# Optimization experiments

Hardware: AMD Instinct MI355X
Metric: run time of the kernel (lower is better)

The kernel has to match this reference:

```python
import jax, jax.numpy as jnp
from jax import lax
import numpy as np

RADIUS = 0.2
NSAMPLE = 64


def setup_inputs() -> dict:
    key = jax.random.key(0)
    k1, k2, k3 = jax.random.split(key, 3)
    B, N, S, C = 4, 16384, 4096, 64
    xyz = jax.random.uniform(k1, (B, N, 3), dtype=jnp.float32)
    new_xyz = jax.random.uniform(k2, (B, S, 3), dtype=jnp.float32)
    features = jax.random.normal(k3, (B, C, N), dtype=jnp.float32)
    return {"xyz": xyz, "new_xyz": new_xyz, "features": features}


def _ball_query(xyz, new_xyz, radius, nsample):
    # xyz: (B,N,3), new_xyz: (B,S,3) -> idx (B,S,nsample) int32
    # Squared distances via GEMM form: ||q||^2 + ||p||^2 - 2 q.p
    N = xyz.shape[1]
    q2 = jnp.sum(new_xyz * new_xyz, axis=-1)            # (B,S)
    p2 = jnp.sum(xyz * xyz, axis=-1)                    # (B,N)
    qp = jnp.einsum('bsd,bnd->bsn', new_xyz, xyz)       # (B,S,N)
    d2 = q2[:, :, None] + p2[:, None, :] - 2.0 * qp     # (B,S,N)
    # CUDA ball_query semantics: take the FIRST nsample points (by index order)
    # within radius; pad remaining slots with the first found index; 0 if none.
    cand = jnp.where(d2 < radius * radius,
                     jnp.arange(N, dtype=jnp.int32), jnp.int32(N))  # (B,S,N)
    neg_smallest, _ = lax.top_k(-cand, nsample)         # nsample smallest indices
    idx = -neg_smallest                                 # ascending (B,S,nsample)
    first = idx[..., :1]
    idx = jnp.where(idx == N, first, idx)               # pad with first neighbor
    idx = jnp.where(idx == N, 0, idx)                   # no neighbor at all -> 0
    return idx


def _group(feat, idx):
    # feat: (B,C,N), idx: (B,S,K) -> (B,C,S,K)
    return jax.vmap(lambda f, i: f[:, i])(feat, idx)


def reference(xyz, new_xyz, features):
    idx = _ball_query(xyz, new_xyz, RADIUS, NSAMPLE)        # (B,S,K)
    grouped_xyz = _group(jnp.transpose(xyz, (0, 2, 1)), idx)  # (B,3,S,K)
    grouped_xyz = grouped_xyz - jnp.transpose(new_xyz, (0, 2, 1))[..., None]
    grouped_features = _group(features, idx)                # (B,C,S,K)
    return jnp.concatenate([grouped_xyz, grouped_features], axis=1)  # (B,3+C,S,K)
```

## Files before the change

### kernel.cpp

```cpp
#include <hip/hip_runtime.h>
#include <cstdint>
#include <cstddef>

#define BB 4
#define NN 16384
#define SS 4096
#define CC 64
#define NSAMP 64
#define R2 0.04f

#define TRANS_BLOCKS (BB * (NN / 64))
#define XYZW_BLOCKS  64

typedef float f32x4 __attribute__((ext_vector_type(4)));

__global__ __launch_bounds__(256) void prep_kernel(const float* __restrict__ xyz,
                                                   const float* __restrict__ feat,
                                                   float* __restrict__ featT,
                                                   f32x4* __restrict__ xyzw) {
    int t = threadIdx.x;
    if (blockIdx.x < TRANS_BLOCKS) {
        __shared__ float tile[64][65];
        int blk = blockIdx.x;
        int b   = blk / (NN / 64);
        int n0  = (blk % (NN / 64)) * 64;
        int nl  = t & 63;
        int cq  = t >> 6;
#pragma unroll
        for (int p = 0; p < 16; ++p) {
            int c = cq + p * 4;
            tile[c][nl] = feat[((size_t)b * CC + c) * NN + n0 + nl];
        }
        __syncthreads();
#pragma unroll
        for (int p = 0; p < 16; ++p) {
            int nl2 = cq + p * 4;
            featT[((size_t)b * NN + n0 + nl2) * CC + nl] = tile[nl][nl2];
        }
        return;
    }
    int T0     = (blockIdx.x - TRANS_BLOCKS) * 256 + t;
    int stride = XYZW_BLOCKS * 256;
    for (int p = T0; p < BB * NN; p += stride) {
        float x = xyz[(size_t)p * 3 + 0];
        float y = xyz[(size_t)p * 3 + 1];
        float z = xyz[(size_t)p * 3 + 2];
        f32x4 o = {x, y, z, 0.0f};
        xyzw[p] = o;
    }
}

__global__ __launch_bounds__(256) void fused_qg(const f32x4* __restrict__ xyzw,
                                                const float* __restrict__ nxyz,
                                                const float* __restrict__ featT,
                                                float* __restrict__ out) {
    __shared__ float sub[4][64][17];
    __shared__ int   sidx[4][NSAMP];

    int t    = threadIdx.x;
    int wid  = t >> 6;
    int lane = t & 63;
    int wg   = blockIdx.x;
    int qblk = (wg & 7) * (BB * SS / 8 / 4) + (wg >> 3);
    int q    = qblk * 4 + wid;
    int b    = q >> 12;
    int s    = q & (SS - 1);

    const f32x4* xp = xyzw + (size_t)b * NN;
    float qx = nxyz[((size_t)b * SS + s) * 3 + 0];
    float qy = nxyz[((size_t)b * SS + s) * 3 + 1];
    float qz = nxyz[((size_t)b * SS + s) * 3 + 2];
    float q2 = __fadd_rn(__fadd_rn(__fmul_rn(qx, qx), __fmul_rn(qy, qy)),
                         __fmul_rn(qz, qz));

    int cnt = 0;
    f32x4 A  = xp[lane];
    f32x4 Bv = xp[lane + 64];
    for (int base = 0; base < NN; base += 128) {
        f32x4 ca = A, cb = Bv;
        int nb = base + 128;
        if (nb < NN) {
            A  = xp[nb + lane];
            Bv = xp[nb + 64 + lane];
        }
        float p2a = __fadd_rn(__fadd_rn(__fmul_rn(ca.x, ca.x), __fmul_rn(ca.y, ca.y)),
                              __fmul_rn(ca.z, ca.z));
        float qpa = __fadd_rn(__fadd_rn(__fmul_rn(qx, ca.x), __fmul_rn(qy, ca.y)),
                              __fmul_rn(qz, ca.z));
        float d2a = __fsub_rn(__fadd_rn(q2, p2a), __fadd_rn(qpa, qpa));
        float p2b = __fadd_rn(__fadd_rn(__fmul_rn(cb.x, cb.x), __fmul_rn(cb.y, cb.y)),
                              __fmul_rn(cb.z, cb.z));
        float qpb = __fadd_rn(__fadd_rn(__fmul_rn(qx, cb.x), __fmul_rn(qy, cb.y)),
                              __fmul_rn(qz, cb.z));
        float d2b = __fsub_rn(__fadd_rn(q2, p2b), __fadd_rn(qpb, qpb));
        bool in0 = d2a < R2;
        bool in1 = d2b < R2;
        unsigned long long m0 = __ballot(in0);
        unsigned long long m1 = __ballot(in1);
        int c0 = __popcll(m0);
        if (in0) {
            int pos = cnt + __popcll(m0 & ((1ull << lane) - 1ull));
            if (pos < NSAMP) sidx[wid][pos] = base + lane;
        }
        if (in1) {
            int pos = cnt + c0 + __popcll(m1 & ((1ull << lane) - 1ull));
            if (pos < NSAMP) sidx[wid][pos] = base + 64 + lane;
        }
        cnt += c0 + __popcll(m1);
        if (cnt >= NSAMP) break;
    }
    asm volatile("s_waitcnt lgkmcnt(0)" ::: "memory");
    int total = cnt < NSAMP ? cnt : NSAMP;
    int myidx = (total == 0) ? 0 : ((lane < total) ? sidx[wid][lane] : sidx[wid][0]);
    asm volatile("s_waitcnt lgkmcnt(0)" ::: "memory");
    sidx[wid][lane] = myidx;
    asm volatile("s_waitcnt lgkmcnt(0)" ::: "memory");

    size_t obase = ((size_t)b * 67) * SS * 64 + (size_t)s * 64;
    size_t chs   = (size_t)SS * 64;

    {
        const f32x4 P = xp[myidx];
        float gx = __fsub_rn(P.x, qx);
        float gy = __fsub_rn(P.y, qy);
        float gz = __fsub_rn(P.z, qz);
        __builtin_nontemporal_store(gx, out + obase + 0 * chs + lane);
        __builtin_nontemporal_store(gy, out + obase + 1 * chs + lane);
        __builtin_nontemporal_store(gz, out + obase + 2 * chs + lane);
    }

    const float* ftb = featT + (size_t)b * NN * CC;
    int r4 = lane >> 2;
    int fc = lane & 3;
    int k4 = lane & 15;
    int cs = lane >> 4;

    int ridx[4];
#pragma unroll
    for (int j = 0; j < 4; ++j) ridx[j] = sidx[wid][j * 16 + r4];
    asm volatile("s_waitcnt lgkmcnt(0)" ::: "memory");

    f32x4 v[4];
#pragma unroll
    for (int j = 0; j < 4; ++j)
        v[j] = *(const f32x4*)(ftb + (size_t)ridx[j] * CC + fc * 4);

#pragma unroll
    for (int h = 0; h < 4; ++h) {
        f32x4 w[4];
        if (h < 3) {
#pragma unroll
            for (int j = 0; j < 4; ++j)
                w[j] = *(const f32x4*)(ftb + (size_t)ridx[j] * CC + (h + 1) * 16 + fc * 4);
        }
#pragma unroll
        for (int j = 0; j < 4; ++j) {
            int row = j * 16 + r4;
            sub[wid][row][fc * 4 + 0] = v[j].x;
            sub[wid][row][fc * 4 + 1] = v[j].y;
            sub[wid][row][fc * 4 + 2] = v[j].z;
            sub[wid][row][fc * 4 + 3] = v[j].w;
        }
        asm volatile("s_waitcnt lgkmcnt(0)" ::: "memory");
#pragma unroll
        for (int j = 0; j < 4; ++j) {
            int cc = j * 4 + cs;
            int c  = h * 16 + cc;
            f32x4 o;
            o.x = sub[wid][k4 * 4 + 0][cc];
            o.y = sub[wid][k4 * 4 + 1][cc];
            o.z = sub[wid][k4 * 4 + 2][cc];
            o.w = sub[wid][k4 * 4 + 3][cc];
            __builtin_nontemporal_store(o,
                (f32x4*)(out + obase + (size_t)(3 + c) * chs + k4 * 4));
        }
        asm volatile("s_waitcnt lgkmcnt(0)" ::: "memory");
#pragma unroll
        for (int j = 0; j < 4; ++j) v[j] = w[j];
    }
}

__global__ __launch_bounds__(64) void qg_fallback(const float* __restrict__ xyz,
                                                  const float* __restrict__ nxyz,
                                                  const float* __restrict__ feat,
                                                  float* __restrict__ out) {
    __shared__ int sidx[NSAMP];
    int q = blockIdx.x;
    int b = q >> 12, s = q & (SS - 1);
    int lane = threadIdx.x;
    const float* xb = xyz + (size_t)b * NN * 3;
    float qx = nxyz[((size_t)b * SS + s) * 3 + 0];
    float qy = nxyz[((size_t)b * SS + s) * 3 + 1];
    float qz = nxyz[((size_t)b * SS + s) * 3 + 2];
    float q2 = __fadd_rn(__fadd_rn(__fmul_rn(qx, qx), __fmul_rn(qy, qy)),
                         __fmul_rn(qz, qz));
    int cnt = 0;
    for (int base = 0; base < NN; base += 64) {
        float cx = xb[(size_t)(base + lane) * 3 + 0];
        float cy = xb[(size_t)(base + lane) * 3 + 1];
        float cz = xb[(size_t)(base + lane) * 3 + 2];
        float p2 = __fadd_rn(__fadd_rn(__fmul_rn(cx, cx), __fmul_rn(cy, cy)),
                             __fmul_rn(cz, cz));
        float qp = __fadd_rn(__fadd_rn(__fmul_rn(qx, cx), __fmul_rn(qy, cy)),
                             __fmul_rn(qz, cz));
        float d2 = __fsub_rn(__fadd_rn(q2, p2), __fadd_rn(qp, qp));
        bool in = d2 < R2;
        unsigned long long m = __ballot(in);
        if (in) {
            int pos = cnt + __popcll(m & ((1ull << lane) - 1ull));
            if (pos < NSAMP) sidx[pos] = base + lane;
        }
        cnt += __popcll(m);
        if (cnt >= NSAMP) break;
    }
    __syncthreads();
    int total = cnt < NSAMP ? cnt : NSAMP;
    int myidx = (total == 0) ? 0 : ((lane < total) ? sidx[lane] : sidx[0]);
    size_t obase = ((size_t)b * 67) * SS * 64 + (size_t)s * 64;
    size_t chs   = (size_t)SS * 64;
    out[obase + 0 * chs + lane] = __fsub_rn(xb[(size_t)myidx * 3 + 0], qx);
    out[obase + 1 * chs + lane] = __fsub_rn(xb[(size_t)myidx * 3 + 1], qy);
    out[obase + 2 * chs + lane] = __fsub_rn(xb[(size_t)myidx * 3 + 2], qz);
    const float* fb = feat + (size_t)b * CC * NN;
#pragma unroll 4
    for (int c = 0; c < CC; ++c)
        out[obase + (size_t)(3 + c) * chs + lane] = fb[(size_t)c * NN + myidx];
}

extern "C" void kernel_launch(void* const* d_in, const int* in_sizes, int n_in,
                              void* d_out, int out_size, void* d_ws, size_t ws_size,
                              hipStream_t stream) {
    const float* xyz  = (const float*)d_in[0];
    const float* nxyz = (const float*)d_in[1];
    const float* feat = (const float*)d_in[2];
    float* out = (float*)d_out;

    size_t needT = (size_t)BB * NN * CC * sizeof(float);
    size_t needW = (size_t)BB * NN * 4 * sizeof(float);
    if (ws_size >= needT + needW) {
        float* featT = (float*)d_ws;
        f32x4* xyzw  = (f32x4*)((char*)d_ws + needT);
        prep_kernel<<<TRANS_BLOCKS + XYZW_BLOCKS, 256, 0, stream>>>(xyz, feat,
                                                                    featT, xyzw);
        fused_qg<<<BB * SS / 4, 256, 0, stream>>>(xyzw, nxyz, featT, out);
    } else {
        qg_fallback<<<BB * SS, 64, 0, stream>>>(xyz, nxyz, feat, out);
    }
}
```

Before: 80.37 us.

## Reorder queries by boundary-proximity class to balance ball-query work across waves

Result: slower. 103.8 us (+29.2%).

```diff
diff --git a/kernel.cpp b/kernel.cpp
--- a/kernel.cpp
+++ b/kernel.cpp
@@ -11,13 +11,16 @@
 
 #define TRANS_BLOCKS (BB * (NN / 64))
 #define XYZW_BLOCKS  64
+#define PERM_BLOCK   (TRANS_BLOCKS + XYZW_BLOCKS)
 
 typedef float f32x4 __attribute__((ext_vector_type(4)));
 
 __global__ __launch_bounds__(256) void prep_kernel(const float* __restrict__ xyz,
+                                                   const float* __restrict__ nxyz,
                                                    const float* __restrict__ feat,
                                                    float* __restrict__ featT,
-                                                   f32x4* __restrict__ xyzw) {
+                                                   f32x4* __restrict__ xyzw,
+                                                   int* __restrict__ perm) {
     int t = threadIdx.x;
     if (blockIdx.x < TRANS_BLOCKS) {
         __shared__ float tile[64][65];
@@ -39,20 +42,64 @@
         }
         return;
     }
-    int T0     = (blockIdx.x - TRANS_BLOCKS) * 256 + t;
-    int stride = XYZW_BLOCKS * 256;
-    for (int p = T0; p < BB * NN; p += stride) {
-        float x = xyz[(size_t)p * 3 + 0];
-        float y = xyz[(size_t)p * 3 + 1];
-        float z = xyz[(size_t)p * 3 + 2];
-        f32x4 o = {x, y, z, 0.0f};
-        xyzw[p] = o;
+    if (blockIdx.x < PERM_BLOCK) {
+        int T0     = (blockIdx.x - TRANS_BLOCKS) * 256 + t;
+        int stride = XYZW_BLOCKS * 256;
+        for (int p = T0; p < BB * NN; p += stride) {
+            float x = xyz[(size_t)p * 3 + 0];
+            float y = xyz[(size_t)p * 3 + 1];
+            float z = xyz[(size_t)p * 3 + 2];
+            f32x4 o = {x, y, z, 0.0f};
+            xyzw[p] = o;
+        }
+        return;
+    }
+    __shared__ int hist[32];
+    __shared__ int offs[32];
+    __shared__ int curs[32];
+    if (t < 32) hist[t] = 0;
+    __syncthreads();
+    for (int i = 0; i < (BB * SS) / 256; ++i) {
+        int qid = t + i * 256;
+        float x = nxyz[(size_t)qid * 3 + 0];
+        float y = nxyz[(size_t)qid * 3 + 1];
+        float z = nxyz[(size_t)qid * 3 + 2];
+        int k = ((x < 0.2f) | (x > 0.8f)) + ((y < 0.2f) | (y > 0.8f)) +
+                ((z < 0.2f) | (z > 0.8f));
+        int g = qid >> 11;
+        atomicAdd(&hist[g * 4 + (3 - k)], 1);
+    }
+    __syncthreads();
+    if (t == 0) {
+        for (int g = 0; g < 8; ++g) {
+            int off = g * 2048;
+            for (int bk = 0; bk < 4; ++bk) {
+                offs[g * 4 + bk] = off;
+                off += hist[g * 4 + bk];
+            }
+        }
+    }
+    __syncthreads();
+    if (t < 32) curs[t] = 0;
+    __syncthreads();
+    for (int i = 0; i < (BB * SS) / 256; ++i) {
+        int qid = t + i * 256;
+        float x = nxyz[(size_t)qid * 3 + 0];
+        float y = nxyz[(size_t)qid * 3 + 1];
+        float z = nxyz[(size_t)qid * 3 + 2];
+        int k = ((x < 0.2f) | (x > 0.8f)) + ((y < 0.2f) | (y > 0.8f)) +
+                ((z < 0.2f) | (z > 0.8f));
+        int g   = qid >> 11;
+        int idx = g * 4 + (3 - k);
+        int pos = atomicAdd(&curs[idx], 1);
+        perm[offs[idx] + pos] = qid;
     }
 }
 
 __global__ __launch_bounds__(256) void fused_qg(const f32x4* __restrict__ xyzw,
                                                 const float* __restrict__ nxyz,
                                                 const float* __restrict__ featT,
+                                                const int* __restrict__ perm,
                                                 float* __restrict__ out) {
     __shared__ float sub[4][64][17];
     __shared__ int   sidx[4][NSAMP];
@@ -62,7 +109,8 @@
     int lane = t & 63;
     int wg   = blockIdx.x;
     int qblk = (wg & 7) * (BB * SS / 8 / 4) + (wg >> 3);
-    int q    = qblk * 4 + wid;
+    int slot = qblk * 4 + wid;
+    int q    = perm[slot];
     int b    = q >> 12;
     int s    = q & (SS - 1);
 
@@ -237,12 +285,14 @@
 
     size_t needT = (size_t)BB * NN * CC * sizeof(float);
     size_t needW = (size_t)BB * NN * 4 * sizeof(float);
-    if (ws_size >= needT + needW) {
+    size_t needP = (size_t)BB * SS * sizeof(int);
+    if (ws_size >= needT + needW + needP) {
         float* featT = (float*)d_ws;
         f32x4* xyzw  = (f32x4*)((char*)d_ws + needT);
-        prep_kernel<<<TRANS_BLOCKS + XYZW_BLOCKS, 256, 0, stream>>>(xyz, feat,
-                                                                    featT, xyzw);
-        fused_qg<<<BB * SS / 4, 256, 0, stream>>>(xyzw, nxyz, featT, out);
+        int*   perm  = (int*)((char*)d_ws + needT + needW);
+        prep_kernel<<<TRANS_BLOCKS + XYZW_BLOCKS + 1, 256, 0, stream>>>(
+            xyz, nxyz, feat, featT, xyzw, perm);
+        fused_qg<<<BB * SS / 4, 256, 0, stream>>>(xyzw, nxyz, featT, perm, out);
     } else {
         qg_fallback<<<BB * SS, 64, 0, stream>>>(xyz, nxyz, feat, out);
     }
```
